# Kernel tuning notes

Measured on AMD Instinct MI355X. Metric: run time of the kernel, lower is better.

Reference implementation:

```python
import jax, jax.numpy as jnp
import numpy as np

D_K = 64  # per-head key dim, used for 1/sqrt(d_k) scaling

def setup_inputs() -> dict:
    key = jax.random.key(0)
    ks = jax.random.split(key, 5)
    B, S, D, H, DK, DV = 4, 2048, 1024, 16, 64, 64
    # xavier_normal-ish scale for [D, DK] weights
    w_std = float(np.sqrt(2.0 / (D + DK)))
    return {
        "x":  jax.random.normal(ks[0], (B, S, D), dtype=jnp.float32),
        "W_Q": jax.random.normal(ks[1], (H, D, DK), dtype=jnp.float32) * w_std,
        "W_K": jax.random.normal(ks[2], (H, D, DK), dtype=jnp.float32) * w_std,
        "W_V": jax.random.normal(ks[3], (H, D, DV), dtype=jnp.float32) * w_std,
        "W_O": jax.random.normal(ks[4], (H * DV, D), dtype=jnp.float32) * float(np.sqrt(1.0 / (H * DV))),
    }

def reference(x, W_Q, W_K, W_V, W_O):
    # x: [B,S,D]; W_Q/W_K/W_V: [H,D,Dk]; W_O: [H*Dv, D]
    q = jnp.einsum("bsd,hdk->bhsk", x, W_Q)
    k = jnp.einsum("bsd,hdk->bhsk", x, W_K)
    v = jnp.einsum("bsd,hdv->bhsv", x, W_V)
    scale = 1.0 / jnp.sqrt(jnp.asarray(D_K, dtype=x.dtype))
    scores = jnp.einsum("bhsk,bhtk->bhst", q, k) * scale  # [B,H,S,S]
    weights = jax.nn.softmax(scores, axis=-1)
    out = jnp.einsum("bhst,bhtv->bhsv", weights, v)       # [B,H,S,Dv]
    B, H, S, DV = out.shape
    # concat heads in order head0..headH-1 along last dim, matching slice writes
    attn_out = jnp.transpose(out, (0, 2, 1, 3)).reshape(B, S, H * DV)
    return attn_out @ W_O
```

## Files before the change

### kernel.cpp

```cpp
#include <hip/hip_runtime.h>
#include <hip/hip_bf16.h>
#include <math.h>

#define BB 4
#define SS 2048
#define DD 1024
#define HH 16
#define DKV 64

typedef __attribute__((ext_vector_type(8))) short bf16x8;
typedef __attribute__((ext_vector_type(4))) float f32x4;
typedef __attribute__((ext_vector_type(2))) __fp16 f16x2;
typedef __attribute__((ext_vector_type(4))) __fp16 f16x4;
typedef unsigned short u16;
typedef unsigned int u32;

__device__ inline u16 f2bf(float f) {
  union { float f; u32 u; } v; v.f = f;
  u32 r = v.u + 0x7FFFu + ((v.u >> 16) & 1u);
  return (u16)(r >> 16);
}
__device__ inline u32 pack2bf(float a, float b) {
  return (u32)f2bf(a) | ((u32)f2bf(b) << 16);
}
__device__ inline u32 pack2h(float a, float b) {
  union { f16x2 h; u32 u; } c;
  c.h = __builtin_amdgcn_cvt_pkrtz(a, b);
  return c.u;
}
__device__ inline void gload16(const u16* g, u16* l) {
  __builtin_amdgcn_global_load_lds(
      (const __attribute__((address_space(1))) u32*)g,
      (__attribute__((address_space(3))) u32*)l, 16, 0, 0);
}

__global__ __launch_bounds__(256) void cvt_x(const float* __restrict__ x,
                                             u16* __restrict__ xb) {
  const long i = ((long)blockIdx.x * 256 + threadIdx.x) * 4;
  const float4 v = *(const float4*)&x[i];
  uint2 o = {pack2bf(v.x, v.y), pack2bf(v.z, v.w)};
  *(uint2*)&xb[i] = o;
}

__global__ __launch_bounds__(256) void wqkv_trans(
    const float* __restrict__ Wq, const float* __restrict__ Wk,
    const float* __restrict__ Wv, u16* __restrict__ Wt) {
  __shared__ u16 T[64][65];
  const int z = blockIdx.z;
  const int which = z >> 4, h = z & 15;
  const float* inb =
      (which == 0 ? Wq : (which == 1 ? Wk : Wv)) + (long)h * DD * DKV;
  u16* outb = Wt + (long)which * DD * DD + (long)h * DKV * DD;
  const int r0 = blockIdx.x * 64;
  const int t = threadIdx.x;
  const int r = t >> 2, cc = (t & 3) * 16;
#pragma unroll
  for (int j = 0; j < 16; j += 4) {
    const float4 v = *(const float4*)&inb[(long)(r0 + r) * DKV + cc + j];
    T[cc + j + 0][r] = f2bf(v.x);
    T[cc + j + 1][r] = f2bf(v.y);
    T[cc + j + 2][r] = f2bf(v.z);
    T[cc + j + 3][r] = f2bf(v.w);
  }
  __syncthreads();
  const int c = t >> 2, rr = (t & 3) * 16;
  u16 tmp[16];
#pragma unroll
  for (int j = 0; j < 16; ++j) tmp[j] = T[c][rr + j];
  *(uint4*)&outb[(long)c * DD + r0 + rr] = *(uint4*)&tmp[0];
  *(uint4*)&outb[(long)c * DD + r0 + rr + 8] = *(uint4*)&tmp[8];
}

__global__ __launch_bounds__(256) void wo_trans(const float* __restrict__ in,
                                                u16* __restrict__ out) {
  __shared__ u16 T[64][65];
  const int r0 = blockIdx.x * 64, c0 = blockIdx.y * 64;
  const int t = threadIdx.x;
  const int r = t >> 2, cc = (t & 3) * 16;
#pragma unroll
  for (int j = 0; j < 16; j += 4) {
    const float4 v = *(const float4*)&in[(long)(r0 + r) * DD + c0 + cc + j];
    T[cc + j + 0][r] = f2bf(v.x);
    T[cc + j + 1][r] = f2bf(v.y);
    T[cc + j + 2][r] = f2bf(v.z);
    T[cc + j + 3][r] = f2bf(v.w);
  }
  __syncthreads();
  const int c = t >> 2, rr = (t & 3) * 16;
  u16 tmp[16];
#pragma unroll
  for (int j = 0; j < 16; ++j) tmp[j] = T[c][rr + j];
  *(uint4*)&out[(long)(c0 + c) * DD + r0 + rr] = *(uint4*)&tmp[0];
  *(uint4*)&out[(long)(c0 + c) * DD + r0 + rr + 8] = *(uint4*)&tmp[8];
}

__global__ __launch_bounds__(256) void gemm_qkv(
    const u16* __restrict__ xb, const u16* __restrict__ Wt,
    u16* __restrict__ Q, u16* __restrict__ K, u16* __restrict__ Vt) {
  __shared__ u16 Xs[128][32];
  __shared__ u16 Ws[128][32];
  const int tid = threadIdx.x;
  const int wv = tid >> 6, lane = tid & 63;
  const int quad = lane >> 4, ln = lane & 15;
  const int m0 = blockIdx.x * 128, n0 = blockIdx.y * 128;
  const int mbase = (wv & 1) * 64, nbase = (wv >> 1) * 64;
  f32x4 zero = {0.f, 0.f, 0.f, 0.f};
  f32x4 acc[4][4];
#pragma unroll
  for (int a = 0; a < 4; ++a)
#pragma unroll
    for (int b = 0; b < 4; ++b) acc[a][b] = zero;
  const int srow = wv * 32 + (lane >> 2);
  const int ch = (lane & 3) * 8;
  const u16* gx0 = &xb[(long)(m0 + srow) * DD + ch];
  const u16* gx1 = &xb[(long)(m0 + srow + 16) * DD + ch];
  const u16* gw0 = &Wt[(long)(n0 + srow) * DD + ch];
  const u16* gw1 = &Wt[(long)(n0 + srow + 16) * DD + ch];
  u16* lx0 = &Xs[wv * 32][0];
  u16* lx1 = &Xs[wv * 32 + 16][0];
  u16* lw0 = &Ws[wv * 32][0];
  u16* lw1 = &Ws[wv * 32 + 16][0];
  const int which = n0 >> 10;
  if (which < 2) {
    for (int kt = 0; kt < DD; kt += 32) {
      __syncthreads();
      gload16(gx0, lx0);
      gload16(gx1, lx1);
      gload16(gw0, lw0);
      gload16(gw1, lw1);
      gx0 += 32; gx1 += 32; gw0 += 32; gw1 += 32;
      __syncthreads();
      bf16x8 a[4], b[4];
#pragma unroll
      for (int g = 0; g < 4; ++g) {
        a[g] = *(const bf16x8*)&Xs[mbase + g * 16 + ln][quad * 8];
        b[g] = *(const bf16x8*)&Ws[nbase + g * 16 + ln][quad * 8];
      }
#pragma unroll
      for (int mg = 0; mg < 4; ++mg)
#pragma unroll
        for (int ng = 0; ng < 4; ++ng)
          acc[mg][ng] = __builtin_amdgcn_mfma_f32_16x16x32_bf16(
              b[ng], a[mg], acc[mg][ng], 0, 0, 0);
    }
    const float qs = 0.18033688011112042f;
    u16* O = which == 0 ? Q : K;
    const float sc = which == 0 ? qs : 1.0f;
#pragma unroll
    for (int mg = 0; mg < 4; ++mg) {
      const int m = m0 + mbase + mg * 16 + ln;
      const int b_ = m >> 11, s_ = m & (SS - 1);
#pragma unroll
      for (int ng = 0; ng < 4; ++ng) {
        const int rem = (n0 + nbase + ng * 16 + quad * 4) & 1023;
        const int h = rem >> 6, nv = rem & 63;
        const long off = (((long)b_ * HH + h) * SS + s_) * DKV + nv;
        const f32x4 v = acc[mg][ng];
        uint2 o = {pack2bf(v[0] * sc, v[1] * sc), pack2bf(v[2] * sc, v[3] * sc)};
        *(uint2*)&O[off] = o;
      }
    }
  } else {
    for (int kt = 0; kt < DD; kt += 32) {
      __syncthreads();
      gload16(gx0, lx0);
      gload16(gx1, lx1);
      gload16(gw0, lw0);
      gload16(gw1, lw1);
      gx0 += 32; gx1 += 32; gw0 += 32; gw1 += 32;
      __syncthreads();
      bf16x8 a[4], b[4];
#pragma unroll
      for (int g = 0; g < 4; ++g) {
        a[g] = *(const bf16x8*)&Xs[mbase + g * 16 + ln][quad * 8];
        b[g] = *(const bf16x8*)&Ws[nbase + g * 16 + ln][quad * 8];
      }
#pragma unroll
      for (int mg = 0; mg < 4; ++mg)
#pragma unroll
        for (int ng = 0; ng < 4; ++ng)
          acc[mg][ng] = __builtin_amdgcn_mfma_f32_16x16x32_bf16(
              a[mg], b[ng], acc[mg][ng], 0, 0, 0);
    }
#pragma unroll
    for (int mg = 0; mg < 4; ++mg) {
      const int m = m0 + mbase + mg * 16 + quad * 4;
      const int b_ = m >> 11, s_ = m & (SS - 1);
#pragma unroll
      for (int ng = 0; ng < 4; ++ng) {
        const int rem = (n0 + nbase + ng * 16 + ln) & 1023;
        const int h = rem >> 6, nv = rem & 63;
        const f32x4 v = acc[mg][ng];
        uint2 o = {pack2h(v[0], v[1]), pack2h(v[2], v[3])};
        *(uint2*)&Vt[(((long)b_ * HH + h) * DKV + nv) * SS + s_] = o;
      }
    }
  }
}

__global__ __launch_bounds__(256) void attn_mfma(
    const u16* Qg, const u16* __restrict__ Kg, const u16* __restrict__ Vtg,
    u16* Og) {
  __shared__ u16 Ks[64][72];
  __shared__ u16 Vs[64][140];
  const int tid = threadIdx.x;
  const int wv = tid >> 6, lane = tid & 63;
  const int quad = lane >> 4, ln = lane & 15;
  const long base = (long)blockIdx.y * SS * DKV;
  const int s0 = blockIdx.x * 256;
  bf16x8 qf[4][2];
#pragma unroll
  for (int qg = 0; qg < 4; ++qg)
#pragma unroll
    for (int ks = 0; ks < 2; ++ks)
      qf[qg][ks] = *(const bf16x8*)&Qg[base +
          (long)(s0 + wv * 64 + qg * 16 + ln) * DKV + ks * 32 + quad * 8];
  f32x4 zero = {0.f, 0.f, 0.f, 0.f};
  f32x4 minus8 = {-8.f, -8.f, -8.f, -8.f};
  f32x4 of[4][4];
#pragma unroll
  for (int qg = 0; qg < 4; ++qg)
#pragma unroll
    for (int dvg = 0; dvg < 4; ++dvg) of[qg][dvg] = zero;
  float lp[4] = {0.f, 0.f, 0.f, 0.f};
  const int sr = tid >> 2, sc0 = (tid & 3) * 16;
  for (int t0 = 0; t0 < SS; t0 += 64) {
    const uint4 kv0 = *(const uint4*)&Kg[base + (long)(t0 + sr) * DKV + sc0];
    const uint4 kv1 = *(const uint4*)&Kg[base + (long)(t0 + sr) * DKV + sc0 + 8];
    const uint4 vv0 = *(const uint4*)&Vtg[base + (long)sr * SS + t0 + sc0];
    const uint4 vv1 = *(const uint4*)&Vtg[base + (long)sr * SS + t0 + sc0 + 8];
    __syncthreads();
    *(uint4*)&Ks[sr][sc0] = kv0;
    *(uint4*)&Ks[sr][sc0 + 8] = kv1;
    {
      uint2 lo0 = {vv0.x, vv0.y}, hi0 = {vv0.z, vv0.w};
      uint2 lo1 = {vv1.x, vv1.y}, hi1 = {vv1.z, vv1.w};
      *(uint2*)&Vs[sr][sc0] = lo0;
      *(uint2*)&Vs[sr][sc0 + 4] = hi0;
      *(uint2*)&Vs[sr][sc0 + 8] = lo1;
      *(uint2*)&Vs[sr][sc0 + 12] = hi1;
    }
    __syncthreads();
    f16x4 pb[4][4];
#pragma unroll
    for (int kg = 0; kg < 4; ++kg) {
      bf16x8 kf0 = *(const bf16x8*)&Ks[kg * 16 + ln][quad * 8];
      bf16x8 kf1 = *(const bf16x8*)&Ks[kg * 16 + ln][32 + quad * 8];
#pragma unroll
      for (int qg = 0; qg < 4; ++qg) {
        f32x4 st = minus8;
        st = __builtin_amdgcn_mfma_f32_16x16x32_bf16(kf0, qf[qg][0], st, 0, 0, 0);
        st = __builtin_amdgcn_mfma_f32_16x16x32_bf16(kf1, qf[qg][1], st, 0, 0, 0);
        f32x4 p;
#pragma unroll
        for (int i = 0; i < 4; ++i) p[i] = __builtin_amdgcn_exp2f(st[i]);
        lp[qg] += (p[0] + p[1]) + (p[2] + p[3]);
        const f16x2 lo = __builtin_amdgcn_cvt_pkrtz(p[0], p[1]);
        const f16x2 hi = __builtin_amdgcn_cvt_pkrtz(p[2], p[3]);
        pb[kg][qg] = __builtin_shufflevector(lo, hi, 0, 1, 2, 3);
      }
    }
#pragma unroll
    for (int dvg = 0; dvg < 4; ++dvg) {
      f16x4 vf[4];
#pragma unroll
      for (int kg = 0; kg < 4; ++kg)
        vf[kg] = *(const f16x4*)&Vs[dvg * 16 + ln][kg * 16 + quad * 4];
#pragma unroll
      for (int qg = 0; qg < 4; ++qg)
#pragma unroll
        for (int kg = 0; kg < 4; ++kg)
          of[qg][dvg] = __builtin_amdgcn_mfma_f32_16x16x16f16(
              vf[kg], pb[kg][qg], of[qg][dvg], 0, 0, 0);
    }
  }
#pragma unroll
  for (int qg = 0; qg < 4; ++qg) {
    float l = lp[qg];
    l += __shfl_xor(l, 16);
    l += __shfl_xor(l, 32);
    const float inv = 1.f / l;
    const long row = base + (long)(s0 + wv * 64 + qg * 16 + ln) * DKV;
#pragma unroll
    for (int dvg = 0; dvg < 4; ++dvg) {
      const f32x4 v = of[qg][dvg];
      uint2 o = {pack2bf(v[0] * inv, v[1] * inv), pack2bf(v[2] * inv, v[3] * inv)};
      *(uint2*)&Og[row + dvg * 16 + quad * 4] = o;
    }
  }
}

__global__ __launch_bounds__(256) void gemm_out(
    const u16* __restrict__ A, const u16* __restrict__ Wot,
    float* __restrict__ out) {
  __shared__ u16 Xs[128][32];
  __shared__ u16 Ws[128][32];
  const int tid = threadIdx.x;
  const int wv = tid >> 6, lane = tid & 63;
  const int quad = lane >> 4, ln = lane & 15;
  const int m0 = blockIdx.x * 128, n0 = blockIdx.y * 128;
  const int mbase = (wv & 1) * 64, nbase = (wv >> 1) * 64;
  f32x4 zero = {0.f, 0.f, 0.f, 0.f};
  f32x4 acc[4][4];
#pragma unroll
  for (int a = 0; a < 4; ++a)
#pragma unroll
    for (int b = 0; b < 4; ++b) acc[a][b] = zero;
  const int srow = wv * 32 + (lane >> 2);
  const int ch = (lane & 3) * 8;
  const int am0 = m0 + srow, am1 = m0 + srow + 16;
  const long ac0 = ((long)(am0 >> 11) * HH) * SS * DKV + (long)(am0 & (SS - 1)) * DKV;
  const long ac1 = ((long)(am1 >> 11) * HH) * SS * DKV + (long)(am1 & (SS - 1)) * DKV;
  const u16* gw0 = &Wot[(long)(n0 + srow) * DD + ch];
  const u16* gw1 = &Wot[(long)(n0 + srow + 16) * DD + ch];
  u16* lx0 = &Xs[wv * 32][0];
  u16* lx1 = &Xs[wv * 32 + 16][0];
  u16* lw0 = &Ws[wv * 32][0];
  u16* lw1 = &Ws[wv * 32 + 16][0];
  for (int kt = 0; kt < DD; kt += 32) {
    const long hoff = (long)(kt >> 6) * SS * DKV + (kt & 63) + ch;
    __syncthreads();
    gload16(&A[ac0 + hoff], lx0);
    gload16(&A[ac1 + hoff], lx1);
    gload16(gw0, lw0);
    gload16(gw1, lw1);
    gw0 += 32; gw1 += 32;
    __syncthreads();
    bf16x8 a[4], b[4];
#pragma unroll
    for (int g = 0; g < 4; ++g) {
      a[g] = *(const bf16x8*)&Xs[mbase + g * 16 + ln][quad * 8];
      b[g] = *(const bf16x8*)&Ws[nbase + g * 16 + ln][quad * 8];
    }
#pragma unroll
    for (int mg = 0; mg < 4; ++mg)
#pragma unroll
      for (int ng = 0; ng < 4; ++ng)
        acc[mg][ng] = __builtin_amdgcn_mfma_f32_16x16x32_bf16(
            b[ng], a[mg], acc[mg][ng], 0, 0, 0);
  }
#pragma unroll
  for (int mg = 0; mg < 4; ++mg) {
    const long row = (long)(m0 + mbase + mg * 16 + ln) * DD;
#pragma unroll
    for (int ng = 0; ng < 4; ++ng)
      *(f32x4*)&out[row + n0 + nbase + ng * 16 + quad * 4] = acc[mg][ng];
  }
}

extern "C" void kernel_launch(void* const* d_in, const int* in_sizes, int n_in,
                              void* d_out, int out_size, void* d_ws, size_t ws_size,
                              hipStream_t stream) {
  const float* x  = (const float*)d_in[0];
  const float* Wq = (const float*)d_in[1];
  const float* Wk = (const float*)d_in[2];
  const float* Wv = (const float*)d_in[3];
  const float* Wo = (const float*)d_in[4];
  float* out = (float*)d_out;
  u16* xb  = (u16*)d_ws;
  u16* Wt  = xb + (size_t)8192 * 1024;
  u16* Wot = Wt + (size_t)3072 * 1024;
  u16* Q   = Wot + (size_t)1024 * 1024;
  u16* K   = Q + (size_t)BB * HH * SS * DKV;
  u16* Vt  = K + (size_t)BB * HH * SS * DKV;
  const dim3 blk(256);
  cvt_x<<<dim3(8192), blk, 0, stream>>>(x, xb);
  wqkv_trans<<<dim3(16, 1, 48), blk, 0, stream>>>(Wq, Wk, Wv, Wt);
  wo_trans<<<dim3(16, 16), blk, 0, stream>>>(Wo, Wot);
  gemm_qkv<<<dim3(64, 24), blk, 0, stream>>>(xb, Wt, Q, K, Vt);
  attn_mfma<<<dim3(8, 64), blk, 0, stream>>>(Q, K, Vt, Q);
  gemm_out<<<dim3(64, 8), blk, 0, stream>>>(Q, Wot, out);
}
```

Measured before the change: 297.8 us.

## Use 16x16x32 f16 MFMA for PV with permlane fragment reshuffle and register prefetch

Replaces the 16x16x16 f16 MFMAs in the P·V product with 16x16x32 f16 MFMAs, halving the MFMA instruction count. Because the wider MFMA needs a different register layout, the probability fragments from pairs of key groups are rearranged across lanes with permlane32/permlane16 swaps. K/V tiles for the next step are now loaded from global memory into registers right after the barrier, so the loads overlap with compute. Launch bounds are set to ask for two blocks per CU. The cost is extra cross-lane permute instructions and higher register pressure.

```diff
diff --git a/kernel.cpp b/kernel.cpp
--- a/kernel.cpp
+++ b/kernel.cpp
@@ -12,8 +12,10 @@
 typedef __attribute__((ext_vector_type(4))) float f32x4;
 typedef __attribute__((ext_vector_type(2))) __fp16 f16x2;
 typedef __attribute__((ext_vector_type(4))) __fp16 f16x4;
+typedef __attribute__((ext_vector_type(8))) __fp16 f16x8;
 typedef unsigned short u16;
 typedef unsigned int u32;
+typedef __attribute__((ext_vector_type(2))) unsigned int u32x2;
 
 __device__ inline u16 f2bf(float f) {
   union { float f; u32 u; } v; v.f = f;
@@ -32,6 +34,31 @@
   __builtin_amdgcn_global_load_lds(
       (const __attribute__((address_space(1))) u32*)g,
       (__attribute__((address_space(3))) u32*)l, 16, 0, 0);
+}
+
+__device__ inline void pl32(u32 a, u32 b, u32& x, u32& y) {
+#if __has_builtin(__builtin_amdgcn_permlane32_swap)
+  u32x2 r = __builtin_amdgcn_permlane32_swap(a, b, false, false);
+  x = r.x; y = r.y;
+#else
+  const bool hi = (threadIdx.x & 32) != 0;
+  u32 as = (u32)__shfl_xor((int)a, 32);
+  u32 bs = (u32)__shfl_xor((int)b, 32);
+  x = hi ? bs : a;
+  y = hi ? b : as;
+#endif
+}
+__device__ inline void pl16(u32 a, u32 b, u32& x, u32& y) {
+#if __has_builtin(__builtin_amdgcn_permlane16_swap)
+  u32x2 r = __builtin_amdgcn_permlane16_swap(a, b, false, false);
+  x = r.x; y = r.y;
+#else
+  const bool odd = (threadIdx.x & 16) != 0;
+  u32 as = (u32)__shfl_xor((int)a, 16);
+  u32 bs = (u32)__shfl_xor((int)b, 16);
+  x = odd ? bs : a;
+  y = odd ? b : as;
+#endif
 }
 
 __global__ __launch_bounds__(256) void cvt_x(const float* __restrict__ x,
@@ -198,7 +225,7 @@
   }
 }
 
-__global__ __launch_bounds__(256) void attn_mfma(
+__global__ __launch_bounds__(256, 2) void attn_mfma(
     const u16* Qg, const u16* __restrict__ Kg, const u16* __restrict__ Vtg,
     u16* Og) {
   __shared__ u16 Ks[64][72];
@@ -224,11 +251,13 @@
     for (int dvg = 0; dvg < 4; ++dvg) of[qg][dvg] = zero;
   float lp[4] = {0.f, 0.f, 0.f, 0.f};
   const int sr = tid >> 2, sc0 = (tid & 3) * 16;
+  const u16* gk = &Kg[base + (long)sr * DKV + sc0];
+  const u16* gv = &Vtg[base + (long)sr * SS + sc0];
+  uint4 kv0 = *(const uint4*)gk;
+  uint4 kv1 = *(const uint4*)(gk + 8);
+  uint4 vv0 = *(const uint4*)gv;
+  uint4 vv1 = *(const uint4*)(gv + 8);
   for (int t0 = 0; t0 < SS; t0 += 64) {
-    const uint4 kv0 = *(const uint4*)&Kg[base + (long)(t0 + sr) * DKV + sc0];
-    const uint4 kv1 = *(const uint4*)&Kg[base + (long)(t0 + sr) * DKV + sc0 + 8];
-    const uint4 vv0 = *(const uint4*)&Vtg[base + (long)sr * SS + t0 + sc0];
-    const uint4 vv1 = *(const uint4*)&Vtg[base + (long)sr * SS + t0 + sc0 + 8];
     __syncthreads();
     *(uint4*)&Ks[sr][sc0] = kv0;
     *(uint4*)&Ks[sr][sc0 + 8] = kv1;
@@ -241,37 +270,65 @@
       *(uint2*)&Vs[sr][sc0 + 12] = hi1;
     }
     __syncthreads();
-    f16x4 pb[4][4];
-#pragma unroll
-    for (int kg = 0; kg < 4; ++kg) {
-      bf16x8 kf0 = *(const bf16x8*)&Ks[kg * 16 + ln][quad * 8];
-      bf16x8 kf1 = *(const bf16x8*)&Ks[kg * 16 + ln][32 + quad * 8];
+    if (t0 + 64 < SS) {
+      gk += 64 * DKV;
+      gv += 64;
+      kv0 = *(const uint4*)gk;
+      kv1 = *(const uint4*)(gk + 8);
+      vv0 = *(const uint4*)gv;
+      vv1 = *(const uint4*)(gv + 8);
+    }
+#pragma unroll
+    for (int half = 0; half < 2; ++half) {
+      f16x4 pe[4], po[4];
+#pragma unroll
+      for (int sub = 0; sub < 2; ++sub) {
+        const int kg = half * 2 + sub;
+        bf16x8 kf0 = *(const bf16x8*)&Ks[kg * 16 + ln][quad * 8];
+        bf16x8 kf1 = *(const bf16x8*)&Ks[kg * 16 + ln][32 + quad * 8];
+#pragma unroll
+        for (int qg = 0; qg < 4; ++qg) {
+          f32x4 st = minus8;
+          st = __builtin_amdgcn_mfma_f32_16x16x32_bf16(kf0, qf[qg][0], st, 0, 0, 0);
+          st = __builtin_amdgcn_mfma_f32_16x16x32_bf16(kf1, qf[qg][1], st, 0, 0, 0);
+          f32x4 p;
+#pragma unroll
+          for (int i = 0; i < 4; ++i) p[i] = __builtin_amdgcn_exp2f(st[i]);
+          lp[qg] += (p[0] + p[1]) + (p[2] + p[3]);
+          const f16x2 lo = __builtin_amdgcn_cvt_pkrtz(p[0], p[1]);
+          const f16x2 hi = __builtin_amdgcn_cvt_pkrtz(p[2], p[3]);
+          const f16x4 fr = __builtin_shufflevector(lo, hi, 0, 1, 2, 3);
+          if (sub == 0) pe[qg] = fr; else po[qg] = fr;
+        }
+      }
+      f16x8 pb2[4];
 #pragma unroll
       for (int qg = 0; qg < 4; ++qg) {
-        f32x4 st = minus8;
-        st = __builtin_amdgcn_mfma_f32_16x16x32_bf16(kf0, qf[qg][0], st, 0, 0, 0);
-        st = __builtin_amdgcn_mfma_f32_16x16x32_bf16(kf1, qf[qg][1], st, 0, 0, 0);
-        f32x4 p;
-#pragma unroll
-        for (int i = 0; i < 4; ++i) p[i] = __builtin_amdgcn_exp2f(st[i]);
-        lp[qg] += (p[0] + p[1]) + (p[2] + p[3]);
-        const f16x2 lo = __builtin_amdgcn_cvt_pkrtz(p[0], p[1]);
-        const f16x2 hi = __builtin_amdgcn_cvt_pkrtz(p[2], p[3]);
-        pb[kg][qg] = __builtin_shufflevector(lo, hi, 0, 1, 2, 3);
-      }
-    }
-#pragma unroll
-    for (int dvg = 0; dvg < 4; ++dvg) {
-      f16x4 vf[4];
-#pragma unroll
-      for (int kg = 0; kg < 4; ++kg)
-        vf[kg] = *(const f16x4*)&Vs[dvg * 16 + ln][kg * 16 + quad * 4];
-#pragma unroll
-      for (int qg = 0; qg < 4; ++qg)
-#pragma unroll
-        for (int kg = 0; kg < 4; ++kg)
-          of[qg][dvg] = __builtin_amdgcn_mfma_f32_16x16x16f16(
-              vf[kg], pb[kg][qg], of[qg][dvg], 0, 0, 0);
+        union { f16x4 h; u32 d[2]; } E, O;
+        E.h = pe[qg]; O.h = po[qg];
+        u32 dw0, dw1, dw2, dw3;
+        {
+          u32 x, y; pl32(E.d[0], O.d[0], x, y);
+          pl16(x, y, dw0, dw2);
+        }
+        {
+          u32 x, y; pl32(E.d[1], O.d[1], x, y);
+          pl16(x, y, dw1, dw3);
+        }
+        union { u32 d[4]; f16x8 h; } R;
+        R.d[0] = dw0; R.d[1] = dw1; R.d[2] = dw2; R.d[3] = dw3;
+        pb2[qg] = R.h;
+      }
+#pragma unroll
+      for (int dvg = 0; dvg < 4; ++dvg) {
+        const f16x4 v0 = *(const f16x4*)&Vs[dvg * 16 + ln][half * 32 + quad * 8];
+        const f16x4 v1 = *(const f16x4*)&Vs[dvg * 16 + ln][half * 32 + quad * 8 + 4];
+        const f16x8 vf = __builtin_shufflevector(v0, v1, 0, 1, 2, 3, 4, 5, 6, 7);
+#pragma unroll
+        for (int qg = 0; qg < 4; ++qg)
+          of[qg][dvg] = __builtin_amdgcn_mfma_f32_16x16x32_f16(
+              vf, pb2[qg], of[qg][dvg], 0, 0, 0);
+      }
     }
   }
 #pragma unroll
```

Measured after the change: 267.0 us. -10.3%, faster.
